# Kernel optimization log

Hardware: AMD Instinct MI355X
Metric: run time of the kernel (lower is better)

Reference implementation:

```python
import jax, jax.numpy as jnp
import numpy as np
import math

CHANNELS = 128
NUM_NODES = 170
LENGTH = 12
BATCH = 128


def setup_inputs() -> dict:
    key = jax.random.key(0)
    k_x, k_es = jax.random.split(key)
    x = jax.random.normal(k_x, (BATCH, CHANNELS, NUM_NODES, LENGTH), dtype=jnp.float32)
    # xavier_uniform for E_s [channels, num_nodes]
    bound = math.sqrt(6.0 / (CHANNELS + NUM_NODES))
    E_s = jax.random.uniform(k_es, (CHANNELS, NUM_NODES), dtype=jnp.float32,
                             minval=-bound, maxval=bound)
    return {"x": x, "E_s": E_s}


def reference(x, E_s):
    # x: [B, C, N, T], E_s: [C, M] with M == N (num_nodes)
    # Note: the original also computes E_t = x * E_tod**2, which is dead code
    # (never used in the returned value), so it is omitted here.
    C = x.shape[1]
    # node embeddings: sum over channel and time -> [B, N, M]
    E_d = jnp.tanh(jnp.einsum('bcnt,cm->bnm', x, E_s))
    # node-node similarity: contract over the M (embedding) axis -> [B, N, N]
    scores = jax.nn.relu(jnp.einsum('bnm,bkm->bnk', E_d, E_d) / jnp.sqrt(jnp.float32(C)))
    A_adp = jax.nn.softmax(scores, axis=-1)  # [B, N, N]
    A_mean = A_adp.mean(axis=0)              # [N, N]
    return (A_mean > 0.5).astype(jnp.float32)
```

## Files before the change

### kernel.cpp

```cpp
#include <hip/hip_runtime.h>
#include <math.h>

#define NB 128
#define NC 128
#define NN 170
#define NT 12
#define NP 192
#define MP 176

#define EST_SZ ((size_t)NP * NC)
#define P_SZ   ((size_t)NB * NN * MP)

typedef _Float16 h8 __attribute__((ext_vector_type(8)));
typedef float    f4 __attribute__((ext_vector_type(4)));

__device__ __forceinline__ float fast_tanh(float x) {
    float cx = fminf(fmaxf(x, -15.f), 15.f);
    float e  = __expf(2.f * cx);
    return (e - 1.f) * __builtin_amdgcn_rcpf(e + 1.f);
}

__global__ __launch_bounds__(256) void kprep_est(const float* __restrict__ Es,
                                                 _Float16* __restrict__ Est) {
    int idx = blockIdx.x * 256 + threadIdx.x;
    int m = idx >> 7, c = idx & 127;
    Est[idx] = (m < NN) ? (_Float16)Es[c * NN + m] : (_Float16)0.f;
}

#define ATSW(row, c)  ((row) * 128 + (((((c) >> 3) ^ ((row) & 7)) << 3) | ((c) & 7)))
#define EDSW(row, m)  ((row) * 192 + (((((m) >> 3) ^ ((row) & 7)) << 3) | ((m) & 7)))
#define SCSTR 204

__global__ __launch_bounds__(1024) void kA_fused(const float* __restrict__ x,
                                                 const _Float16* __restrict__ Est,
                                                 _Float16* __restrict__ P) {
    const int h = blockIdx.x, b = blockIdx.y;
    const int r0 = h * 96;
    const int t = threadIdx.x;
    const int lane = t & 63, wave = t >> 6;
    const int l15 = lane & 15, quad = lane >> 4;
    const int wr = wave >> 2, wc = wave & 3;

    __shared__ __align__(16) char     UN[192 * 128 * 2];
    __shared__ __align__(16) _Float16 EdL[192 * 192];
    _Float16* At = (_Float16*)UN;
    float*    Sc = (float*)UN;

    const float* __restrict__ xb = x + (size_t)b * NC * NN * NT;
    #pragma unroll
    for (int p = 0; p < 24; ++p) {
        int g3 = p * 16 + wave;
        int c  = g3 / 3;
        int ng = g3 - c * 3;
        int n  = ng * 64 + lane;
        float sv = 0.f;
        if (n < NN) {
            const float4* q = reinterpret_cast<const float4*>(
                xb + ((size_t)c * NN + n) * NT);
            float4 a0 = q[0], a1 = q[1], a2 = q[2];
            sv = ((a0.x + a0.y) + (a0.z + a0.w))
               + ((a1.x + a1.y) + (a1.z + a1.w))
               + ((a2.x + a2.y) + (a2.z + a2.w));
        }
        At[ATSW(n, c)] = (_Float16)sv;
    }
    __syncthreads();

    {
        f4 acc1[3][3] = {};
        #pragma unroll
        for (int kk = 0; kk < 4; ++kk) {
            int ks = kk * 32 + quad * 8;
            h8 a[3], bf[3];
            #pragma unroll
            for (int rt = 0; rt < 3; ++rt) {
                int row = wr * 48 + rt * 16 + l15;
                a[rt] = *reinterpret_cast<const h8*>(
                    &At[row * 128 + (((ks >> 3) ^ (row & 7)) << 3)]);
            }
            #pragma unroll
            for (int ci = 0; ci < 3; ++ci) {
                int m = wc * 48 + ci * 16 + l15;
                bf[ci] = *reinterpret_cast<const h8*>(Est + (size_t)m * NC + ks);
            }
            #pragma unroll
            for (int rt = 0; rt < 3; ++rt)
                #pragma unroll
                for (int ci = 0; ci < 3; ++ci)
                    acc1[rt][ci] = __builtin_amdgcn_mfma_f32_16x16x32_f16(
                        a[rt], bf[ci], acc1[rt][ci], 0, 0, 0);
        }
        #pragma unroll
        for (int rt = 0; rt < 3; ++rt)
            #pragma unroll
            for (int ci = 0; ci < 3; ++ci) {
                int m = wc * 48 + ci * 16 + l15;
                #pragma unroll
                for (int reg = 0; reg < 4; ++reg) {
                    int n = wr * 48 + rt * 16 + quad * 4 + reg;
                    EdL[EDSW(n, m)] = (_Float16)fast_tanh(acc1[rt][ci][reg]);
                }
            }
    }
    __syncthreads();

    f4 acc2[3][3] = {};
    if (wave < 8) {
        const int gr = wave >> 2, gc = wave & 3;
        #pragma unroll 2
        for (int mc = 0; mc < 192; mc += 32) {
            int mg = (mc >> 3) + quad;
            h8 a2[3], b2[3];
            #pragma unroll
            for (int rt = 0; rt < 3; ++rt) {
                int row = r0 + gr * 48 + rt * 16 + l15;
                a2[rt] = *reinterpret_cast<const h8*>(
                    &EdL[row * 192 + ((mg ^ (row & 7)) << 3)]);
            }
            #pragma unroll
            for (int ci = 0; ci < 3; ++ci) {
                int row = gc * 48 + ci * 16 + l15;
                b2[ci] = *reinterpret_cast<const h8*>(
                    &EdL[row * 192 + ((mg ^ (row & 7)) << 3)]);
            }
            #pragma unroll
            for (int rt = 0; rt < 3; ++rt)
                #pragma unroll
                for (int ci = 0; ci < 3; ++ci)
                    acc2[rt][ci] = __builtin_amdgcn_mfma_f32_16x16x32_f16(
                        a2[rt], b2[ci], acc2[rt][ci], 0, 0, 0);
        }
    }

    const float scale = 0.08838834764831845f;
    for (int p = 0; p < 2; ++p) {
        __syncthreads();
        if (wave < 8 && (wave >> 2) == p) {
            const int gc = wave & 3;
            #pragma unroll
            for (int rt = 0; rt < 3; ++rt)
                #pragma unroll
                for (int ci = 0; ci < 3; ++ci) {
                    int col = gc * 48 + ci * 16 + l15;
                    #pragma unroll
                    for (int reg = 0; reg < 4; ++reg) {
                        int rloc = rt * 16 + quad * 4 + reg;
                        Sc[rloc * SCSTR + col] = fmaxf(acc2[rt][ci][reg] * scale, 0.f);
                    }
                }
        }
        __syncthreads();
        #pragma unroll
        for (int rr = 0; rr < 3; ++rr) {
            int r = wave * 3 + rr;
            int n = r0 + p * 48 + r;
            if (n >= NN) continue;
            float v0 = Sc[r * SCSTR + lane];
            float v1 = Sc[r * SCSTR + lane + 64];
            int  k2i = lane + 128;
            bool has2 = (k2i < NN);
            float v2 = has2 ? Sc[r * SCSTR + k2i] : -1.f;
            float m = fmaxf(fmaxf(v0, v1), v2);
            #pragma unroll
            for (int off = 32; off; off >>= 1) m = fmaxf(m, __shfl_xor(m, off, 64));
            float e0 = __expf(v0 - m);
            float e1 = __expf(v1 - m);
            float e2 = has2 ? __expf(v2 - m) : 0.f;
            float s = e0 + e1 + e2;
            #pragma unroll
            for (int off = 32; off; off >>= 1) s += __shfl_xor(s, off, 64);
            float inv = 1.f / s;
            _Float16* Pr = P + ((size_t)(b * NN + n)) * MP;
            Pr[lane]      = (_Float16)(e0 * inv);
            Pr[lane + 64] = (_Float16)(e1 * inv);
            if (has2) Pr[k2i] = (_Float16)(e2 * inv);
        }
    }
}

__global__ __launch_bounds__(256) void k4_mean_thresh(const _Float16* __restrict__ P,
                                                      float* __restrict__ out) {
    int p = blockIdx.x * 256 + threadIdx.x;
    if (p >= NN * NN) return;
    int n = p / NN, k = p - n * NN;
    const _Float16* base = P + (size_t)n * MP + k;
    float s0 = 0.f, s1 = 0.f, s2 = 0.f, s3 = 0.f;
    float s4 = 0.f, s5 = 0.f, s6 = 0.f, s7 = 0.f;
    #pragma unroll
    for (int b = 0; b < NB; b += 8) {
        s0 += (float)base[(size_t)(b + 0) * NN * MP];
        s1 += (float)base[(size_t)(b + 1) * NN * MP];
        s2 += (float)base[(size_t)(b + 2) * NN * MP];
        s3 += (float)base[(size_t)(b + 3) * NN * MP];
        s4 += (float)base[(size_t)(b + 4) * NN * MP];
        s5 += (float)base[(size_t)(b + 5) * NN * MP];
        s6 += (float)base[(size_t)(b + 6) * NN * MP];
        s7 += (float)base[(size_t)(b + 7) * NN * MP];
    }
    float s = ((s0 + s1) + (s2 + s3)) + ((s4 + s5) + (s6 + s7));
    out[p] = (s * (1.f / 128.f) > 0.5f) ? 1.f : 0.f;
}

extern "C" void kernel_launch(void* const* d_in, const int* in_sizes, int n_in,
                              void* d_out, int out_size, void* d_ws, size_t ws_size,
                              hipStream_t stream) {
    const float* x  = (const float*)d_in[0];
    const float* Es = (const float*)d_in[1];
    float* out = (float*)d_out;

    _Float16* Est = (_Float16*)d_ws;
    _Float16* P   = Est + EST_SZ;

    kprep_est<<<96, 256, 0, stream>>>(Es, Est);
    kA_fused<<<dim3(2, 128), 1024, 0, stream>>>(x, Est, P);
    k4_mean_thresh<<<113, 256, 0, stream>>>(P, out);
}
```

Measured before the change: 229.1 us.

## Split time-sum reduction into a wide streaming kernel and shrink fused block

The reduction of x over time moves out of the fused per-batch kernel into a separate 4096-block kernel. That kernel streams x with coalesced float4 loads through LDS and writes a compact fp16 [B,C,192] buffer, and it also builds the transposed E_s. The fused kernel drops from 1024 to 512 threads and reads the small fp16 buffer, with each wave doing twice the MFMA tiles and softmax rows. The goal is to read the 100MB input with far more parallelism than 256 blocks give, at the cost of an extra global round-trip and a kernel launch.

```diff
diff --git a/kernel.cpp b/kernel.cpp
--- a/kernel.cpp
+++ b/kernel.cpp
@@ -7,8 +7,10 @@
 #define NT 12
 #define NP 192
 #define MP 176
+#define XSTR 192
 
 #define EST_SZ ((size_t)NP * NC)
+#define XS_SZ  ((size_t)NB * NC * XSTR)
 #define P_SZ   ((size_t)NB * NN * MP)
 
 typedef _Float16 h8 __attribute__((ext_vector_type(8)));
@@ -20,58 +22,87 @@
     return (e - 1.f) * __builtin_amdgcn_rcpf(e + 1.f);
 }
 
-__global__ __launch_bounds__(256) void kprep_est(const float* __restrict__ Es,
-                                                 _Float16* __restrict__ Est) {
-    int idx = blockIdx.x * 256 + threadIdx.x;
-    int m = idx >> 7, c = idx & 127;
-    Est[idx] = (m < NN) ? (_Float16)Es[c * NN + m] : (_Float16)0.f;
+__global__ __launch_bounds__(256) void k1_tsum_est(const float* __restrict__ x,
+                                                   const float* __restrict__ Es,
+                                                   _Float16* __restrict__ xs,
+                                                   _Float16* __restrict__ Est) {
+    const int bid = blockIdx.x;
+    const int t = threadIdx.x;
+    if (bid < 4096) {
+        const int wave = t >> 6, lane = t & 63;
+        const int bc = bid * 4 + wave;
+        __shared__ __align__(16) float4 S4[4][240];
+        float4* S = S4[wave];
+        const float4* xr = reinterpret_cast<const float4*>(x + (size_t)bc * (NN * NT));
+        _Float16* xsr = xs + (size_t)bc * XSTR;
+        #pragma unroll
+        for (int g = 0; g < 3; ++g) {
+            float4 v[3];
+            #pragma unroll
+            for (int j = 0; j < 3; ++j) {
+                int s = g * 192 + j * 64 + lane;
+                v[j] = (s < 510) ? xr[s] : make_float4(0.f, 0.f, 0.f, 0.f);
+            }
+            #pragma unroll
+            for (int j = 0; j < 3; ++j) {
+                int s = j * 64 + lane;
+                S[s + (s >> 2)] = v[j];
+            }
+            asm volatile("s_waitcnt lgkmcnt(0)" ::: "memory");
+            int s0 = 3 * lane, s1 = s0 + 1, s2 = s0 + 2;
+            float4 a0 = S[s0 + (s0 >> 2)];
+            float4 a1 = S[s1 + (s1 >> 2)];
+            float4 a2 = S[s2 + (s2 >> 2)];
+            float sv = ((a0.x + a0.y) + (a0.z + a0.w))
+                     + ((a1.x + a1.y) + (a1.z + a1.w))
+                     + ((a2.x + a2.y) + (a2.z + a2.w));
+            xsr[g * 64 + lane] = (_Float16)sv;
+            asm volatile("s_waitcnt lgkmcnt(0)" ::: "memory");
+        }
+    } else {
+        int idx = (bid - 4096) * 256 + t;
+        int m = idx >> 7, c = idx & 127;
+        Est[idx] = (m < NN) ? (_Float16)Es[c * NN + m] : (_Float16)0.f;
+    }
 }
 
 #define ATSW(row, c)  ((row) * 128 + (((((c) >> 3) ^ ((row) & 7)) << 3) | ((c) & 7)))
 #define EDSW(row, m)  ((row) * 192 + (((((m) >> 3) ^ ((row) & 7)) << 3) | ((m) & 7)))
 #define SCSTR 204
 
-__global__ __launch_bounds__(1024) void kA_fused(const float* __restrict__ x,
-                                                 const _Float16* __restrict__ Est,
-                                                 _Float16* __restrict__ P) {
+__global__ __launch_bounds__(512) void kB_fused(const _Float16* __restrict__ xs,
+                                                const _Float16* __restrict__ Est,
+                                                _Float16* __restrict__ P) {
     const int h = blockIdx.x, b = blockIdx.y;
     const int r0 = h * 96;
     const int t = threadIdx.x;
     const int lane = t & 63, wave = t >> 6;
     const int l15 = lane & 15, quad = lane >> 4;
-    const int wr = wave >> 2, wc = wave & 3;
 
     __shared__ __align__(16) char     UN[192 * 128 * 2];
     __shared__ __align__(16) _Float16 EdL[192 * 192];
     _Float16* At = (_Float16*)UN;
     float*    Sc = (float*)UN;
 
-    const float* __restrict__ xb = x + (size_t)b * NC * NN * NT;
+    const _Float16* __restrict__ xsb = xs + (size_t)b * NC * XSTR;
     #pragma unroll
-    for (int p = 0; p < 24; ++p) {
-        int g3 = p * 16 + wave;
-        int c  = g3 / 3;
-        int ng = g3 - c * 3;
-        int n  = ng * 64 + lane;
-        float sv = 0.f;
-        if (n < NN) {
-            const float4* q = reinterpret_cast<const float4*>(
-                xb + ((size_t)c * NN + n) * NT);
-            float4 a0 = q[0], a1 = q[1], a2 = q[2];
-            sv = ((a0.x + a0.y) + (a0.z + a0.w))
-               + ((a1.x + a1.y) + (a1.z + a1.w))
-               + ((a2.x + a2.y) + (a2.z + a2.w));
-        }
-        At[ATSW(n, c)] = (_Float16)sv;
+    for (int i = 0; i < 6; ++i) {
+        int idx = t + i * 512;
+        int ng = idx >> 7, c = idx & 127;
+        h8 v = *reinterpret_cast<const h8*>(xsb + (size_t)c * XSTR + ng * 8);
+        #pragma unroll
+        for (int j = 0; j < 8; ++j)
+            At[ATSW(ng * 8 + j, c)] = v[j];
     }
     __syncthreads();
 
     {
-        f4 acc1[3][3] = {};
+        const int wr = wave >> 1, wh = wave & 1;
+        f4 acc1[3][6] = {};
         #pragma unroll
         for (int kk = 0; kk < 4; ++kk) {
             int ks = kk * 32 + quad * 8;
-            h8 a[3], bf[3];
+            h8 a[3], bf[6];
             #pragma unroll
             for (int rt = 0; rt < 3; ++rt) {
                 int row = wr * 48 + rt * 16 + l15;
@@ -79,25 +110,25 @@
                     &At[row * 128 + (((ks >> 3) ^ (row & 7)) << 3)]);
             }
             #pragma unroll
-            for (int ci = 0; ci < 3; ++ci) {
-                int m = wc * 48 + ci * 16 + l15;
+            for (int ci = 0; ci < 6; ++ci) {
+                int m = wh * 96 + ci * 16 + l15;
                 bf[ci] = *reinterpret_cast<const h8*>(Est + (size_t)m * NC + ks);
             }
             #pragma unroll
             for (int rt = 0; rt < 3; ++rt)
                 #pragma unroll
-                for (int ci = 0; ci < 3; ++ci)
+                for (int ci = 0; ci < 6; ++ci)
                     acc1[rt][ci] = __builtin_amdgcn_mfma_f32_16x16x32_f16(
                         a[rt], bf[ci], acc1[rt][ci], 0, 0, 0);
         }
         #pragma unroll
         for (int rt = 0; rt < 3; ++rt)
             #pragma unroll
-            for (int ci = 0; ci < 3; ++ci) {
-                int m = wc * 48 + ci * 16 + l15;
+            for (int ci = 0; ci < 6; ++ci) {
+                int m = (wave & 1) * 96 + ci * 16 + l15;
                 #pragma unroll
                 for (int reg = 0; reg < 4; ++reg) {
-                    int n = wr * 48 + rt * 16 + quad * 4 + reg;
+                    int n = (wave >> 1) * 48 + rt * 16 + quad * 4 + reg;
                     EdL[EDSW(n, m)] = (_Float16)fast_tanh(acc1[rt][ci][reg]);
                 }
             }
@@ -105,7 +136,7 @@
     __syncthreads();
 
     f4 acc2[3][3] = {};
-    if (wave < 8) {
+    {
         const int gr = wave >> 2, gc = wave & 3;
         #pragma unroll 2
         for (int mc = 0; mc < 192; mc += 32) {
@@ -135,7 +166,7 @@
     const float scale = 0.08838834764831845f;
     for (int p = 0; p < 2; ++p) {
         __syncthreads();
-        if (wave < 8 && (wave >> 2) == p) {
+        if ((wave >> 2) == p) {
             const int gc = wave & 3;
             #pragma unroll
             for (int rt = 0; rt < 3; ++rt)
@@ -151,8 +182,8 @@
         }
         __syncthreads();
         #pragma unroll
-        for (int rr = 0; rr < 3; ++rr) {
-            int r = wave * 3 + rr;
+        for (int rr = 0; rr < 6; ++rr) {
+            int r = wave * 6 + rr;
             int n = r0 + p * 48 + r;
             if (n >= NN) continue;
             float v0 = Sc[r * SCSTR + lane];
@@ -209,9 +240,10 @@
     float* out = (float*)d_out;
 
     _Float16* Est = (_Float16*)d_ws;
-    _Float16* P   = Est + EST_SZ;
-
-    kprep_est<<<96, 256, 0, stream>>>(Es, Est);
-    kA_fused<<<dim3(2, 128), 1024, 0, stream>>>(x, Est, P);
+    _Float16* xs  = Est + EST_SZ;
+    _Float16* P   = xs + XS_SZ;
+
+    k1_tsum_est<<<4192, 256, 0, stream>>>(x, Es, xs, Est);
+    kB_fused<<<dim3(2, 128), 512, 0, stream>>>(xs, Est, P);
     k4_mean_thresh<<<113, 256, 0, stream>>>(P, out);
 }
```

New measurement: 235.9 us. 1.03x slower.
